# Optimization experiments

Hardware: AMD Instinct MI355X
Metric: run time of the kernel (lower is better)

Reference implementation:

```python
import jax, jax.numpy as jnp
import numpy as np

DIM = 1024
NUM_HEADS = 16
HEAD_DIM = DIM // NUM_HEADS
EPS = 1e-5


def layernorm(x, scale, bias):
    # LayerNorm over the last (head_dim) axis
    mu = jnp.mean(x, axis=-1, keepdims=True)
    var = jnp.var(x, axis=-1, keepdims=True)
    return (x - mu) * jax.lax.rsqrt(var + EPS) * scale + bias


def rope(q):
    # q: [B, H, S, Hd]; standard rotate-half RoPE over head_dim
    S, Hd = q.shape[-2], q.shape[-1]
    inv_freq = 1.0 / (10000.0 ** (jnp.arange(0, Hd, 2, dtype=jnp.float32) / Hd))
    ang = jnp.arange(S, dtype=jnp.float32)[:, None] * inv_freq  # [S, Hd/2]
    cos, sin = jnp.cos(ang), jnp.sin(ang)
    q1, q2 = jnp.split(q, 2, axis=-1)
    return jnp.concatenate([q1 * cos - q2 * sin, q1 * sin + q2 * cos], axis=-1)


def setup_inputs() -> dict:
    key = jax.random.key(0)
    ks = jax.random.split(key, 8)
    B, S, S_ctx = 4, 2048, 2048
    s = 0.02
    return {
        "x": jax.random.normal(ks[0], (B, S, DIM), dtype=jnp.float32),
        "context": jax.random.normal(ks[1], (B, S_ctx, DIM), dtype=jnp.float32),
        "q_w": jax.random.normal(ks[2], (DIM, DIM), dtype=jnp.float32) * s,
        "kv_w": jax.random.normal(ks[3], (DIM, 2 * DIM), dtype=jnp.float32) * s,
        "qn_scale": jnp.ones((HEAD_DIM,), jnp.float32),
        "qn_bias": jnp.zeros((HEAD_DIM,), jnp.float32),
        "kn_scale": jnp.ones((HEAD_DIM,), jnp.float32),
        "kn_bias": jnp.zeros((HEAD_DIM,), jnp.float32),
        "proj_w": jax.random.normal(ks[4], (DIM, DIM), dtype=jnp.float32) * s,
        "proj_b": jnp.zeros((DIM,), jnp.float32),
    }


def reference(x, context, q_w, kv_w, qn_scale, qn_bias, kn_scale, kn_bias, proj_w, proj_b):
    B, S, C = x.shape
    S_ctx = context.shape[1]
    H, Hd = NUM_HEADS, HEAD_DIM
    # projections (no bias: qkv_bias=False)
    q = (x @ q_w).reshape(B, S, H, Hd).transpose(0, 2, 1, 3)        # [B,H,S,Hd]
    kv = (context @ kv_w).reshape(B, S_ctx, 2, H, Hd)
    k = kv[:, :, 0].transpose(0, 2, 1, 3)                           # [B,H,Sc,Hd]
    v = kv[:, :, 1].transpose(0, 2, 1, 3)
    # per-head LayerNorm on q and k
    q = layernorm(q, qn_scale, qn_bias)
    k = layernorm(k, kn_scale, kn_bias)
    # RoPE on q only (as in the original forward)
    q = rope(q)
    # SDPA (eval path: no mask, no dropout)
    scale = 1.0 / jnp.sqrt(jnp.float32(Hd))
    logits = jnp.einsum("bhsd,bhtd->bhst", q, k) * scale
    attn = jax.nn.softmax(logits, axis=-1)
    out = jnp.einsum("bhst,bhtd->bhsd", attn, v)                    # [B,H,S,Hd]
    out = out.transpose(0, 2, 1, 3).reshape(B, S, C)
    return out @ proj_w + proj_b
```

## Files before the change

kernel.cpp:

```cpp
#include <hip/hip_runtime.h>
#include <hip/hip_bf16.h>


typedef short bf16x8 __attribute__((ext_vector_type(8)));
typedef float f32x4 __attribute__((ext_vector_type(4)));

__device__ __forceinline__ short f2s(float f) {
    __hip_bfloat16 h = __float2bfloat16(f);
    return __builtin_bit_cast(short, h);
}

__device__ __forceinline__ f32x4 mfma16(bf16x8 a, bf16x8 b, f32x4 c) {
    return __builtin_amdgcn_mfma_f32_16x16x32_bf16(a, b, c, 0, 0, 0);
}

__device__ __forceinline__ void gload16(short* lds, const short* g) {
    __builtin_amdgcn_global_load_lds((const __attribute__((address_space(1))) void*)g,
                                     (__attribute__((address_space(3))) void*)lds,
                                     16, 0, 0);
}

__device__ __forceinline__ void drain_barrier() {
    asm volatile("s_waitcnt vmcnt(0) lgkmcnt(0)" ::: "memory");
    __syncthreads();
}

__device__ __forceinline__ unsigned int fbits(float f) {
    return __builtin_bit_cast(unsigned int, f);
}

__global__ __launch_bounds__(256) void conv_to_bf16(const float* __restrict__ x,
                                                    const float* __restrict__ ctx,
                                                    short* __restrict__ xb,
                                                    short* __restrict__ cb) {
    const size_t NV = 2097152;
    size_t i = (size_t)blockIdx.x * 256 + threadIdx.x;
    const float4* src = (i < NV) ? (const float4*)x : (const float4*)ctx;
    short* dst = (i < NV) ? xb : cb;
    size_t idx = (i < NV) ? i : i - NV;
    float4 v = src[idx];
    short4 o;
    o.x = f2s(v.x); o.y = f2s(v.y); o.z = f2s(v.z); o.w = f2s(v.w);
    ((short4*)dst)[idx] = o;
}

__global__ __launch_bounds__(256) void transpose_weights(
    const float* __restrict__ q_w, const float* __restrict__ kv_w,
    const float* __restrict__ proj_w,
    short* __restrict__ WqT, short* __restrict__ WkvT, short* __restrict__ WpT) {
    __shared__ float t[32][33];
    const float* src; short* dst; int ld, coff;
    switch (blockIdx.z) {
        case 0:  src = q_w;    dst = WqT;                 ld = 1024; coff = 0;    break;
        case 1:  src = kv_w;   dst = WkvT;                ld = 2048; coff = 0;    break;
        case 2:  src = kv_w;   dst = WkvT + 1024 * 1024;  ld = 2048; coff = 1024; break;
        default: src = proj_w; dst = WpT;                 ld = 1024; coff = 0;    break;
    }
    int n0 = blockIdx.x * 32, k0 = blockIdx.y * 32;
    int tx = threadIdx.x & 31, ty = threadIdx.x >> 5;
    #pragma unroll
    for (int j = 0; j < 32; j += 8)
        t[ty + j][tx] = src[(size_t)(k0 + ty + j) * ld + coff + n0 + tx];
    __syncthreads();
    #pragma unroll
    for (int j = 0; j < 32; j += 8)
        dst[(size_t)(n0 + ty + j) * 1024 + k0 + tx] = f2s(t[tx][ty + j]);
}

__global__ __launch_bounds__(256, 3) void gemm_qkv(
    const short* __restrict__ A,
    const short* __restrict__ Bt,
    const short* __restrict__ A2,
    const short* __restrict__ Bt2,
    const float* __restrict__ qn_scale, const float* __restrict__ qn_bias,
    const float* __restrict__ kn_scale, const float* __restrict__ kn_bias,
    short* __restrict__ outQ, short* __restrict__ outK, short* __restrict__ outV) {
    __shared__ short smem[24576];
    const int tid = threadIdx.x;
    const int w = tid >> 6, lane = tid & 63, quad = lane >> 4, l15 = lane & 15;
    const int wr = w & 1, wc = w >> 1;
    const int m0 = blockIdx.x * 128;

    const int y = blockIdx.y;
    const bool qpath = (y < 8);
    const int n0 = qpath ? y * 128 : (y - 8) * 128;
    const short* Ab = qpath ? A : A2;
    const short* Bb = qpath ? Bt : Bt2;
    const float* lns = qpath ? qn_scale : kn_scale;
    const float* lnb = qpath ? qn_bias : kn_bias;
    const bool vpath = (!qpath) && (n0 >= 1024);

    const int srow = lane >> 2, slot = lane & 3;
    const int kslot = (slot ^ ((srow >> 1) & 3)) * 8;
    const short* Ag0 = Ab + (size_t)(m0 + w * 32 + srow) * 1024 + kslot;
    const short* Ag1 = Ag0 + (size_t)16 * 1024;
    const short* Bg0 = Bb + (size_t)(n0 + w * 32 + srow) * 1024 + kslot;
    const short* Bg1 = Bg0 + (size_t)16 * 1024;
    short* Al = smem + w * 1024;
    short* Bl = smem + 4096 + w * 1024;

    f32x4 acc[4][4];
    #pragma unroll
    for (int r = 0; r < 4; r++)
        #pragma unroll
        for (int c = 0; c < 4; c++) acc[r][c] = f32x4{0.f, 0.f, 0.f, 0.f};

    const int rsw = (l15 >> 1) & 3;
    const int rch = (quad ^ rsw) * 8;

    gload16(Al,              Ag0);
    gload16(Al + 512,        Ag1);
    gload16(Bl,              Bg0);
    gload16(Bl + 512,        Bg1);
    gload16(Al + 8192,       Ag0 + 32);
    gload16(Al + 8192 + 512, Ag1 + 32);
    gload16(Bl + 8192,       Bg0 + 32);
    gload16(Bl + 8192 + 512, Bg1 + 32);
    asm volatile("s_waitcnt vmcnt(4) lgkmcnt(0)" ::: "memory");
    __builtin_amdgcn_s_barrier();

    int curo = 0;
    int pfo = 16384;
    #pragma unroll 1
    for (int t = 0; t < 32; t++) {
        if (t < 30) {
            const int k0 = (t + 2) * 32;
            gload16(Al + pfo,       Ag0 + k0);
            gload16(Al + pfo + 512, Ag1 + k0);
            gload16(Bl + pfo,       Bg0 + k0);
            gload16(Bl + pfo + 512, Bg1 + k0);
        }
        bf16x8 af[4], bfr[4];
        #pragma unroll
        for (int rt = 0; rt < 4; rt++)
            af[rt] = *(const bf16x8*)(smem + curo + (wr * 64 + rt * 16 + l15) * 32 + rch);
        #pragma unroll
        for (int ct = 0; ct < 4; ct++)
            bfr[ct] = *(const bf16x8*)(smem + curo + 4096 + (wc * 64 + ct * 16 + l15) * 32 + rch);
        #pragma unroll
        for (int rt = 0; rt < 4; rt++)
            #pragma unroll
            for (int ct = 0; ct < 4; ct++)
                acc[rt][ct] = mfma16(af[rt], bfr[ct], acc[rt][ct]);
        if (t < 30) {
            asm volatile("s_waitcnt vmcnt(4) lgkmcnt(0)" ::: "memory");
        } else {
            asm volatile("s_waitcnt vmcnt(0) lgkmcnt(0)" ::: "memory");
        }
        __builtin_amdgcn_s_barrier();
        curo += 8192; if (curo == 24576) curo = 0;
        pfo  += 8192; if (pfo  == 24576) pfo  = 0;
    }

    if (!vpath) {
        #pragma unroll
        for (int rt = 0; rt < 4; rt++) {
            #pragma unroll
            for (int i = 0; i < 4; i++) {
                float s = acc[rt][0][i] + acc[rt][1][i] + acc[rt][2][i] + acc[rt][3][i];
                float q = acc[rt][0][i] * acc[rt][0][i] + acc[rt][1][i] * acc[rt][1][i] +
                          acc[rt][2][i] * acc[rt][2][i] + acc[rt][3][i] * acc[rt][3][i];
                #pragma unroll
                for (int off = 1; off < 16; off <<= 1) {
                    s += __shfl_xor(s, off, 64);
                    q += __shfl_xor(q, off, 64);
                }
                float mu = s * (1.f / 64.f);
                float var = q * (1.f / 64.f) - mu * mu;
                float rs = rsqrtf(var + 1e-5f);
                float vals[4];
                #pragma unroll
                for (int ct = 0; ct < 4; ct++) {
                    int hd = ct * 16 + l15;
                    vals[ct] = (acc[rt][ct][i] - mu) * rs * lns[hd] + lnb[hd];
                }
                if (qpath) {
                    int sp = (m0 + wr * 64 + rt * 16 + quad * 4 + i) & 2047;
                    #pragma unroll
                    for (int ct = 0; ct < 2; ct++) {
                        int hd1 = ct * 16 + l15;
                        float ang = (float)sp * exp2f((float)hd1 * (-13.287712379549449f / 32.f));
                        float sn, cs;
                        sincosf(ang, &sn, &cs);
                        float v1 = vals[ct], v2 = vals[ct + 2];
                        vals[ct]     = v1 * cs - v2 * sn;
                        vals[ct + 2] = v1 * sn + v2 * cs;
                    }
                    #pragma unroll
                    for (int ct = 0; ct < 4; ct++) vals[ct] *= 0.1803368801f;
                }
                #pragma unroll
                for (int ct = 0; ct < 4; ct++) acc[rt][ct][i] = vals[ct];
            }
        }
        drain_barrier();
        short* Csm = smem;
        #pragma unroll
        for (int rt = 0; rt < 4; rt++)
            #pragma unroll
            for (int ct = 0; ct < 4; ct++)
                #pragma unroll
                for (int i = 0; i < 4; i++)
                    Csm[(wr * 64 + rt * 16 + quad * 4 + i) * 132 + wc * 64 + ct * 16 + l15] =
                        f2s(acc[rt][ct][i]);
        drain_barrier();
        short* dst = qpath ? outQ : outK;
        #pragma unroll
        for (int it = 0; it < 8; it++) {
            int row = it * 16 + (tid >> 4);
            int chunk = tid & 15;
            bf16x8 v = *(const bf16x8*)(Csm + row * 132 + chunk * 8);
            int hh = ((n0 & 1023) >> 6) + (chunk >> 3);
            int m = m0 + row, b = m >> 11, sp = m & 2047;
            *(bf16x8*)(dst + ((size_t)(b * 16 + hh) * 2048 + sp) * 64 + (chunk & 7) * 8) = v;
        }
    } else {
        const int b = m0 >> 11, h = ((n0 - 1024) >> 6) + wc;
        const int sp = (m0 & 2047) + wr * 64 + quad * 4;
        #pragma unroll
        for (int rt = 0; rt < 4; rt++)
            #pragma unroll
            for (int ct = 0; ct < 4; ct++) {
                short4 pk;
                pk.x = f2s(acc[rt][ct][0]); pk.y = f2s(acc[rt][ct][1]);
                pk.z = f2s(acc[rt][ct][2]); pk.w = f2s(acc[rt][ct][3]);
                int hd = ct * 16 + l15;
                *(short4*)(outV + ((size_t)(b * 16 + h) * 64 + hd) * 2048 + sp + rt * 16) = pk;
            }
    }
}

__global__ __launch_bounds__(256, 3) void gemm_proj_sk(
    const short* __restrict__ A,
    const short* __restrict__ Bt,
    float* __restrict__ partial) {
    __shared__ short smem[24576];
    const int tid = threadIdx.x;
    const int w = tid >> 6, lane = tid & 63, quad = lane >> 4, l15 = lane & 15;
    const int wr = w & 1, wc = w >> 1;
    const int m0 = blockIdx.x * 128, n0 = blockIdx.y * 128;
    const int kz = blockIdx.z;

    const int srow = lane >> 2, slot = lane & 3;
    const int kslot = (slot ^ ((srow >> 1) & 3)) * 8;
    const short* Ag0 = A + (size_t)(m0 + w * 32 + srow) * 1024 + kz * 512 + kslot;
    const short* Ag1 = Ag0 + (size_t)16 * 1024;
    const short* Bg0 = Bt + (size_t)(n0 + w * 32 + srow) * 1024 + kz * 512 + kslot;
    const short* Bg1 = Bg0 + (size_t)16 * 1024;
    short* Al = smem + w * 1024;
    short* Bl = smem + 4096 + w * 1024;

    f32x4 acc[4][4];
    #pragma unroll
    for (int r = 0; r < 4; r++)
        #pragma unroll
        for (int c = 0; c < 4; c++) acc[r][c] = f32x4{0.f, 0.f, 0.f, 0.f};

    const int rsw = (l15 >> 1) & 3;
    const int rch = (quad ^ rsw) * 8;

    gload16(Al,              Ag0);
    gload16(Al + 512,        Ag1);
    gload16(Bl,              Bg0);
    gload16(Bl + 512,        Bg1);
    gload16(Al + 8192,       Ag0 + 32);
    gload16(Al + 8192 + 512, Ag1 + 32);
    gload16(Bl + 8192,       Bg0 + 32);
    gload16(Bl + 8192 + 512, Bg1 + 32);
    asm volatile("s_waitcnt vmcnt(4) lgkmcnt(0)" ::: "memory");
    __builtin_amdgcn_s_barrier();

    int curo = 0;
    int pfo = 16384;
    #pragma unroll 1
    for (int t = 0; t < 16; t++) {
        if (t < 14) {
            const int k0 = (t + 2) * 32;
            gload16(Al + pfo,       Ag0 + k0);
            gload16(Al + pfo + 512, Ag1 + k0);
            gload16(Bl + pfo,       Bg0 + k0);
            gload16(Bl + pfo + 512, Bg1 + k0);
        }
        bf16x8 af[4], bfr[4];
        #pragma unroll
        for (int rt = 0; rt < 4; rt++)
            af[rt] = *(const bf16x8*)(smem + curo + (wr * 64 + rt * 16 + l15) * 32 + rch);
        #pragma unroll
        for (int ct = 0; ct < 4; ct++)
            bfr[ct] = *(const bf16x8*)(smem + curo + 4096 + (wc * 64 + ct * 16 + l15) * 32 + rch);
        #pragma unroll
        for (int rt = 0; rt < 4; rt++)
            #pragma unroll
            for (int ct = 0; ct < 4; ct++)
                acc[rt][ct] = mfma16(af[rt], bfr[ct], acc[rt][ct]);
        if (t < 14) {
            asm volatile("s_waitcnt vmcnt(4) lgkmcnt(0)" ::: "memory");
        } else {
            asm volatile("s_waitcnt vmcnt(0) lgkmcnt(0)" ::: "memory");
        }
        __builtin_amdgcn_s_barrier();
        curo += 8192; if (curo == 24576) curo = 0;
        pfo  += 8192; if (pfo  == 24576) pfo  = 0;
    }

    float* outP = partial + (size_t)kz * 8192 * 1024;
    #pragma unroll
    for (int rt = 0; rt < 4; rt++)
        #pragma unroll
        for (int i = 0; i < 4; i++) {
            size_t m = m0 + wr * 64 + rt * 16 + quad * 4 + i;
            #pragma unroll
            for (int ct = 0; ct < 4; ct++) {
                int n = n0 + wc * 64 + ct * 16 + l15;
                outP[m * 1024 + n] = acc[rt][ct][i];
            }
        }
}

__global__ __launch_bounds__(256) void reduce_bias(
    const float* __restrict__ partial, const float* __restrict__ bias,
    float* __restrict__ out) {
    size_t i = (size_t)blockIdx.x * 256 + threadIdx.x;
    float4 a = ((const float4*)partial)[i];
    float4 b = ((const float4*)(partial + (size_t)8192 * 1024))[i];
    float4 bs = ((const float4*)bias)[i & 255];
    float4 o;
    o.x = a.x + b.x + bs.x; o.y = a.y + b.y + bs.y;
    o.z = a.z + b.z + bs.z; o.w = a.w + b.w + bs.w;
    ((float4*)out)[i] = o;
}

__global__ __launch_bounds__(512, 4) void attn_kernel(
    const short* __restrict__ Q,
    const short* __restrict__ K,
    const short* __restrict__ V,
    short* __restrict__ AO) {
    __shared__ short smem[8192 + 8192 + 8 * 32 * 72];
    const int tid = threadIdx.x;
    const int w = tid >> 6, lane = tid & 63, quad = lane >> 4, l15 = lane & 15;
    const int bh = blockIdx.x, qt = blockIdx.y;
    const short* Qb = Q + (size_t)bh * 2048 * 64;
    const short* Kb = K + (size_t)bh * 2048 * 64;
    const short* Vb = V + (size_t)bh * 64 * 2048;
    short* Pw = smem + 16384 + w * 2304;
    const int q0 = qt * 256 + w * 32;

    const int srow = lane >> 2, slot = lane & 3;
    const int sw = (slot ^ ((srow >> 1) & 3)) * 8;
    const int ws = w & 3;
    const bool kstager = (w < 4);
    const short* Sg = kstager ? (Kb + (size_t)(ws * 16 + srow) * 64 + sw)
                              : (Vb + (size_t)(ws * 16 + srow) * 2048 + sw);
    short* Sl0 = smem + (kstager ? 0 : 8192) + ws * 512;
    const int sstep = kstager ? 4096 : 64;

    bf16x8 bq[2][2];
    #pragma unroll
    for (int nt = 0; nt < 2; nt++)
        #pragma unroll
        for (int ks = 0; ks < 2; ks++)
            bq[nt][ks] = *(const bf16x8*)(Qb + (size_t)(q0 + nt * 16 + l15) * 64 + ks * 32 + quad * 8);

    f32x4 acco[4][2];
    #pragma unroll
    for (int ct = 0; ct < 4; ct++)
        #pragma unroll
        for (int nt = 0; nt < 2; nt++) acco[ct][nt] = f32x4{0.f, 0.f, 0.f, 0.f};
    float lsum[2] = {0.f, 0.f};
    const int rsw = (l15 >> 1) & 3;
    const int rch = (quad ^ rsw) * 8;

    gload16(Sl0,        Sg);
    gload16(Sl0 + 2048, Sg + 32);
    drain_barrier();

    #pragma unroll 1
    for (int t = 0; t < 32; t++) {
        const int cur = (t & 1) * 4096;
        if (t < 31) {
            const int nxt = 4096 - cur;
            gload16(Sl0 + nxt,        Sg + (t + 1) * sstep);
            gload16(Sl0 + nxt + 2048, Sg + (t + 1) * sstep + 32);
        }
        bf16x8 ak[4][2];
        #pragma unroll
        for (int mt = 0; mt < 4; mt++)
            #pragma unroll
            for (int ks = 0; ks < 2; ks++)
                ak[mt][ks] = *(const bf16x8*)(smem + cur + ks * 2048 + (mt * 16 + l15) * 32 + rch);

        #pragma unroll
        for (int mt = 0; mt < 4; mt++) {
            #pragma unroll
            for (int nt = 0; nt < 2; nt++) {
                f32x4 st = f32x4{0.f, 0.f, 0.f, 0.f};
                st = mfma16(ak[mt][0], bq[nt][0], st);
                st = mfma16(ak[mt][1], bq[nt][1], st);
                float e0 = __builtin_amdgcn_exp2f(st[0]);
                float e1 = __builtin_amdgcn_exp2f(st[1]);
                float e2 = __builtin_amdgcn_exp2f(st[2]);
                float e3 = __builtin_amdgcn_exp2f(st[3]);
                lsum[nt] += (e0 + e1) + (e2 + e3);
                unsigned int p01 = __builtin_amdgcn_perm(fbits(e1), fbits(e0), 0x07060302u);
                unsigned int p23 = __builtin_amdgcn_perm(fbits(e3), fbits(e2), 0x07060302u);
                uint2 pw;
                pw.x = p01; pw.y = p23;
                *(uint2*)(Pw + (nt * 16 + l15) * 72 + mt * 16 + quad * 4) = pw;
            }
        }
        asm volatile("" ::: "memory");

        bf16x8 av[4][2];
        #pragma unroll
        for (int ct = 0; ct < 4; ct++)
            #pragma unroll
            for (int ks = 0; ks < 2; ks++)
                av[ct][ks] = *(const bf16x8*)(smem + 8192 + cur + ks * 2048 + (ct * 16 + l15) * 32 + rch);

        bf16x8 bp[2][2];
        #pragma unroll
        for (int nt = 0; nt < 2; nt++)
            #pragma unroll
            for (int ks = 0; ks < 2; ks++)
                bp[nt][ks] = *(const bf16x8*)(Pw + (nt * 16 + l15) * 72 + ks * 32 + quad * 8);
        #pragma unroll
        for (int ct = 0; ct < 4; ct++)
            #pragma unroll
            for (int nt = 0; nt < 2; nt++)
                #pragma unroll
                for (int ks = 0; ks < 2; ks++)
                    acco[ct][nt] = mfma16(av[ct][ks], bp[nt][ks], acco[ct][nt]);
        drain_barrier();
    }

    #pragma unroll
    for (int nt = 0; nt < 2; nt++) {
        lsum[nt] += __shfl_xor(lsum[nt], 16, 64);
        lsum[nt] += __shfl_xor(lsum[nt], 32, 64);
    }
    const int b = bh >> 4, h = bh & 15;
    #pragma unroll
    for (int nt = 0; nt < 2; nt++) {
        float inv = 1.f / lsum[nt];
        int sq = q0 + nt * 16 + l15;
        #pragma unroll
        for (int ct = 0; ct < 4; ct++) {
            short4 pk;
            pk.x = f2s(acco[ct][nt][0] * inv); pk.y = f2s(acco[ct][nt][1] * inv);
            pk.z = f2s(acco[ct][nt][2] * inv); pk.w = f2s(acco[ct][nt][3] * inv);
            *(short4*)(AO + ((size_t)b * 2048 + sq) * 1024 + h * 64 + ct * 16 + quad * 4) = pk;
        }
    }
}

extern "C" void kernel_launch(void* const* d_in, const int* in_sizes, int n_in,
                              void* d_out, int out_size, void* d_ws, size_t ws_size,
                              hipStream_t stream) {
    (void)in_sizes; (void)n_in; (void)out_size; (void)ws_size;
    const float* x      = (const float*)d_in[0];
    const float* ctx    = (const float*)d_in[1];
    const float* q_w    = (const float*)d_in[2];
    const float* kv_w   = (const float*)d_in[3];
    const float* qn_s   = (const float*)d_in[4];
    const float* qn_b   = (const float*)d_in[5];
    const float* kn_s   = (const float*)d_in[6];
    const float* kn_b   = (const float*)d_in[7];
    const float* proj_w = (const float*)d_in[8];
    const float* proj_b = (const float*)d_in[9];
    float* out = (float*)d_out;

    char* ws = (char*)d_ws;
    const size_t MB = 1024 * 1024;
    short* xb   = (short*)(ws + 0 * MB);
    short* cb   = (short*)(ws + 16 * MB);
    short* Qb   = (short*)(ws + 32 * MB);
    short* Kb   = (short*)(ws + 48 * MB);
    short* Vt   = (short*)(ws + 64 * MB);
    short* AO   = (short*)(ws + 80 * MB);
    short* WqT  = (short*)(ws + 96 * MB);
    short* WkvT = (short*)(ws + 98 * MB);
    short* WpT  = (short*)(ws + 102 * MB);
    float* Pp   = (float*)(ws + 0 * MB);

    conv_to_bf16<<<16384, 256, 0, stream>>>(x, ctx, xb, cb);
    transpose_weights<<<dim3(32, 32, 4), 256, 0, stream>>>(q_w, kv_w, proj_w, WqT, WkvT, WpT);
    gemm_qkv<<<dim3(64, 24), 256, 0, stream>>>(xb, WqT, cb, WkvT, qn_s, qn_b, kn_s, kn_b,
                                               Qb, Kb, Vt);
    attn_kernel<<<dim3(64, 8), 512, 0, stream>>>(Qb, Kb, Vt, AO);
    gemm_proj_sk<<<dim3(64, 8, 2), 256, 0, stream>>>(AO, WpT, Pp);
    reduce_bias<<<8192, 256, 0, stream>>>(Pp, proj_b, out);
}
```

Baseline: 323.8 us.

## Drop split-K in projection GEMM, fuse bias, and hoist V loads in attention

```diff
diff --git a/kernel.cpp b/kernel.cpp
--- a/kernel.cpp
+++ b/kernel.cpp
@@ -230,22 +230,22 @@
     }
 }
 
-__global__ __launch_bounds__(256, 3) void gemm_proj_sk(
+__global__ __launch_bounds__(256, 3) void gemm_proj(
     const short* __restrict__ A,
     const short* __restrict__ Bt,
-    float* __restrict__ partial) {
+    float* __restrict__ outF,
+    const float* __restrict__ bias_vec) {
     __shared__ short smem[24576];
     const int tid = threadIdx.x;
     const int w = tid >> 6, lane = tid & 63, quad = lane >> 4, l15 = lane & 15;
     const int wr = w & 1, wc = w >> 1;
     const int m0 = blockIdx.x * 128, n0 = blockIdx.y * 128;
-    const int kz = blockIdx.z;
 
     const int srow = lane >> 2, slot = lane & 3;
     const int kslot = (slot ^ ((srow >> 1) & 3)) * 8;
-    const short* Ag0 = A + (size_t)(m0 + w * 32 + srow) * 1024 + kz * 512 + kslot;
+    const short* Ag0 = A + (size_t)(m0 + w * 32 + srow) * 1024 + kslot;
     const short* Ag1 = Ag0 + (size_t)16 * 1024;
-    const short* Bg0 = Bt + (size_t)(n0 + w * 32 + srow) * 1024 + kz * 512 + kslot;
+    const short* Bg0 = Bt + (size_t)(n0 + w * 32 + srow) * 1024 + kslot;
     const short* Bg1 = Bg0 + (size_t)16 * 1024;
     short* Al = smem + w * 1024;
     short* Bl = smem + 4096 + w * 1024;
@@ -273,8 +273,8 @@
     int curo = 0;
     int pfo = 16384;
     #pragma unroll 1
-    for (int t = 0; t < 16; t++) {
-        if (t < 14) {
+    for (int t = 0; t < 32; t++) {
+        if (t < 30) {
             const int k0 = (t + 2) * 32;
             gload16(Al + pfo,       Ag0 + k0);
             gload16(Al + pfo + 512, Ag1 + k0);
@@ -293,7 +293,7 @@
             #pragma unroll
             for (int ct = 0; ct < 4; ct++)
                 acc[rt][ct] = mfma16(af[rt], bfr[ct], acc[rt][ct]);
-        if (t < 14) {
+        if (t < 30) {
             asm volatile("s_waitcnt vmcnt(4) lgkmcnt(0)" ::: "memory");
         } else {
             asm volatile("s_waitcnt vmcnt(0) lgkmcnt(0)" ::: "memory");
@@ -303,7 +303,6 @@
         pfo  += 8192; if (pfo  == 24576) pfo  = 0;
     }
 
-    float* outP = partial + (size_t)kz * 8192 * 1024;
     #pragma unroll
     for (int rt = 0; rt < 4; rt++)
         #pragma unroll
@@ -312,22 +311,9 @@
             #pragma unroll
             for (int ct = 0; ct < 4; ct++) {
                 int n = n0 + wc * 64 + ct * 16 + l15;
-                outP[m * 1024 + n] = acc[rt][ct][i];
+                outF[m * 1024 + n] = acc[rt][ct][i] + bias_vec[n];
             }
         }
-}
-
-__global__ __launch_bounds__(256) void reduce_bias(
-    const float* __restrict__ partial, const float* __restrict__ bias,
-    float* __restrict__ out) {
-    size_t i = (size_t)blockIdx.x * 256 + threadIdx.x;
-    float4 a = ((const float4*)partial)[i];
-    float4 b = ((const float4*)(partial + (size_t)8192 * 1024))[i];
-    float4 bs = ((const float4*)bias)[i & 255];
-    float4 o;
-    o.x = a.x + b.x + bs.x; o.y = a.y + b.y + bs.y;
-    o.z = a.z + b.z + bs.z; o.w = a.w + b.w + bs.w;
-    ((float4*)out)[i] = o;
 }
 
 __global__ __launch_bounds__(512, 4) void attn_kernel(
@@ -382,12 +368,17 @@
             gload16(Sl0 + nxt,        Sg + (t + 1) * sstep);
             gload16(Sl0 + nxt + 2048, Sg + (t + 1) * sstep + 32);
         }
-        bf16x8 ak[4][2];
+        bf16x8 ak[4][2], av[4][2];
         #pragma unroll
         for (int mt = 0; mt < 4; mt++)
             #pragma unroll
             for (int ks = 0; ks < 2; ks++)
                 ak[mt][ks] = *(const bf16x8*)(smem + cur + ks * 2048 + (mt * 16 + l15) * 32 + rch);
+        #pragma unroll
+        for (int ct = 0; ct < 4; ct++)
+            #pragma unroll
+            for (int ks = 0; ks < 2; ks++)
+                av[ct][ks] = *(const bf16x8*)(smem + 8192 + cur + ks * 2048 + (ct * 16 + l15) * 32 + rch);
 
         #pragma unroll
         for (int mt = 0; mt < 4; mt++) {
@@ -410,19 +401,13 @@
         }
         asm volatile("" ::: "memory");
 
-        bf16x8 av[4][2];
-        #pragma unroll
-        for (int ct = 0; ct < 4; ct++)
-            #pragma unroll
-            for (int ks = 0; ks < 2; ks++)
-                av[ct][ks] = *(const bf16x8*)(smem + 8192 + cur + ks * 2048 + (ct * 16 + l15) * 32 + rch);
-
         bf16x8 bp[2][2];
         #pragma unroll
         for (int nt = 0; nt < 2; nt++)
             #pragma unroll
             for (int ks = 0; ks < 2; ks++)
                 bp[nt][ks] = *(const bf16x8*)(Pw + (nt * 16 + l15) * 72 + ks * 32 + quad * 8);
+        __builtin_amdgcn_s_setprio(1);
         #pragma unroll
         for (int ct = 0; ct < 4; ct++)
             #pragma unroll
@@ -430,6 +415,7 @@
                 #pragma unroll
                 for (int ks = 0; ks < 2; ks++)
                     acco[ct][nt] = mfma16(av[ct][ks], bp[nt][ks], acco[ct][nt]);
+        __builtin_amdgcn_s_setprio(0);
         drain_barrier();
     }
 
@@ -480,13 +466,11 @@
     short* WqT  = (short*)(ws + 96 * MB);
     short* WkvT = (short*)(ws + 98 * MB);
     short* WpT  = (short*)(ws + 102 * MB);
-    float* Pp   = (float*)(ws + 0 * MB);
 
     conv_to_bf16<<<16384, 256, 0, stream>>>(x, ctx, xb, cb);
     transpose_weights<<<dim3(32, 32, 4), 256, 0, stream>>>(q_w, kv_w, proj_w, WqT, WkvT, WpT);
     gemm_qkv<<<dim3(64, 24), 256, 0, stream>>>(xb, WqT, cb, WkvT, qn_s, qn_b, kn_s, kn_b,
                                                Qb, Kb, Vt);
     attn_kernel<<<dim3(64, 8), 512, 0, stream>>>(Qb, Kb, Vt, AO);
-    gemm_proj_sk<<<dim3(64, 8, 2), 256, 0, stream>>>(AO, WpT, Pp);
-    reduce_bias<<<8192, 256, 0, stream>>>(Pp, proj_b, out);
-}
+    gemm_proj<<<dim3(64, 8), 256, 0, stream>>>(AO, WpT, out, proj_b);
+}
```

New measurement: 316.0 us. -2.4%, faster.
